# Performance work log

Hardware: AMD Instinct MI355X
Metric: run time of the kernel (lower is better)

## Reference

```python
import jax, jax.numpy as jnp
import numpy as np

B, S, D, H, F = 2, 2048, 1024, 16, 4096
HD = D // H
EPS = 1e-5
NEG = -1e9


def _layernorm(x, g, b):
    mu = jnp.mean(x, axis=-1, keepdims=True)
    var = jnp.mean((x - mu) ** 2, axis=-1, keepdims=True)
    return (x - mu) * jax.lax.rsqrt(var + EPS) * g + b


def _attention(x, wq, wk, wv, wo, bo):
    b, s, d = x.shape
    q = (x @ wq).reshape(b, s, H, HD).transpose(0, 2, 1, 3)  # [b,h,s,hd]
    k = (x @ wk).reshape(b, s, H, HD).transpose(0, 2, 1, 3)
    v = (x @ wv).reshape(b, s, H, HD).transpose(0, 2, 1, 3)
    scores = jnp.einsum('bhqd,bhkd->bhqk', q, k) / (HD ** 0.5)
    # Faithful to source bug: masked_fill(mask == 0, -1e9) where mask = triu(diag=1)
    # -> positions with k <= q (lower triangle incl. diagonal) are filled with -1e9.
    lower = jnp.tril(jnp.ones((s, s), dtype=bool))
    scores = jnp.where(lower, NEG, scores)
    w = jax.nn.softmax(scores, axis=-1)
    o = jnp.einsum('bhqk,bhkd->bhqd', w, v)
    o = o.transpose(0, 2, 1, 3).reshape(b, s, d)
    return o @ wo + bo


def _ffn(x, w1, b1, w2, b2):
    return jax.nn.gelu(x @ w1 + b1, approximate=False) @ w2 + b2


def setup_inputs() -> dict:
    key = jax.random.key(0)
    ks = jax.random.split(key, 10)
    s = 0.02
    return {
        'x': jax.random.normal(ks[0], (B, S, D), jnp.float32),
        'wq': jax.random.normal(ks[1], (D, D), jnp.float32) * s,
        'wk': jax.random.normal(ks[2], (D, D), jnp.float32) * s,
        'wv': jax.random.normal(ks[3], (D, D), jnp.float32) * s,
        'wo': jax.random.normal(ks[4], (D, D), jnp.float32) * s,
        'bo': jnp.zeros((D,), jnp.float32),
        'ln1_g': jnp.ones((D,), jnp.float32),
        'ln1_b': jnp.zeros((D,), jnp.float32),
        'ln2_g': jnp.ones((D,), jnp.float32),
        'ln2_b': jnp.zeros((D,), jnp.float32),
        'w1': jax.random.normal(ks[5], (D, F), jnp.float32) * s,
        'b1': jnp.zeros((F,), jnp.float32),
        'w2': jax.random.normal(ks[6], (F, D), jnp.float32) * s,
        'b2': jnp.zeros((D,), jnp.float32),
    }


def reference(x, wq, wk, wv, wo, bo, ln1_g, ln1_b, ln2_g, ln2_b, w1, b1, w2, b2):
    shortcut = x
    h = _layernorm(x, ln1_g, ln1_b)
    h = _attention(h, wq, wk, wv, wo, bo)  # dropout = identity (eval)
    h = h + shortcut
    shortcut = h
    h2 = _layernorm(h, ln2_g, ln2_b)
    h2 = _attention(h2, wq, wk, wv, wo, bo)  # same attn module reused, per source
    h2 = _ffn(h2, w1, b1, w2, b2)
    return h2 + shortcut
```

## Files before the change

kernel.cpp:

```cpp
#include <hip/hip_runtime.h>
#include <hip/hip_bf16.h>
#include <math.h>

#define Bz 2
#define Sz 2048
#define Dz 1024
#define Hz 16
#define HDz 64
#define Fz 4096
#define ROWS (Bz*Sz)
#define EPSf 1e-5f
#define NEGf -1e9f
#define SC2f 0.1803368801111204f

typedef __attribute__((ext_vector_type(8))) short short8;
typedef __attribute__((ext_vector_type(4))) float floatx4;

__device__ __forceinline__ unsigned short f2bf(float f){
  __hip_bfloat16 h = __float2bfloat16(f);
  return *(unsigned short*)&h;
}
__device__ __forceinline__ float bf2f(unsigned short u){
  union { unsigned x; float f; } a; a.x = ((unsigned)u) << 16; return a.f;
}

__device__ __forceinline__ float fast_gelu(float x){
  float t  = fabsf(x) * 0.70710678118654752f;
  float kk = __builtin_amdgcn_rcpf(1.0f + 0.3275911f * t);
  float poly = ((((1.061405429f*kk - 1.453152027f)*kk + 1.421413741f)*kk
                 - 0.284496736f)*kk + 0.254829592f)*kk;
  float er = 1.0f - poly * __expf(-t*t);
  er = copysignf(er, x);
  return 0.5f * x * (1.0f + er);
}

__device__ __forceinline__ void gload16(const void* g, void* l){
  __builtin_amdgcn_global_load_lds(
      (const __attribute__((address_space(1))) unsigned int*)g,
      (__attribute__((address_space(3))) unsigned int*)l, 16, 0, 0);
}

__device__ __forceinline__ void bar(){
  asm volatile("" ::: "memory");
  __builtin_amdgcn_s_barrier();
  asm volatile("" ::: "memory");
}
#define WAITV6 asm volatile("s_waitcnt vmcnt(6)" ::: "memory")
#define WAITV0 asm volatile("s_waitcnt vmcnt(0)" ::: "memory")
#define WL0    asm volatile("s_waitcnt lgkmcnt(0)" ::: "memory")

__device__ __forceinline__ void xcd_remap(int& bmblk, int& bnblk){
  int gx = gridDim.x, gy = gridDim.y;
  int id = blockIdx.y * gx + blockIdx.x;
  int xcd = id & 7, local = id >> 3;
  bnblk = local % gx;
  bmblk = xcd * (gy >> 3) + local / gx;
}

__global__ __launch_bounds__(256)
void transpose_cast(const float* __restrict__ W, unsigned short* __restrict__ Wt,
                    int K, int N)
{
  __shared__ unsigned short Ts[32][33];
  int n0 = blockIdx.x*32, k0 = blockIdx.y*32;
  int r = threadIdx.x >> 3, c0 = (threadIdx.x & 7) * 4;
  float4 w4 = *(const float4*)(W + (size_t)(k0+r)*N + n0 + c0);
  Ts[r][c0+0] = f2bf(w4.x); Ts[r][c0+1] = f2bf(w4.y);
  Ts[r][c0+2] = f2bf(w4.z); Ts[r][c0+3] = f2bf(w4.w);
  __syncthreads();
  unsigned v0 = Ts[c0+0][r], v1 = Ts[c0+1][r], v2 = Ts[c0+2][r], v3 = Ts[c0+3][r];
  uint2 p; p.x = v0 | (v1<<16); p.y = v2 | (v3<<16);
  *(uint2*)(Wt + (size_t)(n0+r)*K + k0 + c0) = p;
}

__global__ __launch_bounds__(256)
void transpose_bf(const unsigned short* __restrict__ V, unsigned short* __restrict__ VT)
{
  __shared__ unsigned short Ts[32][33];
  int st = blockIdx.x*32;
  int R0 = blockIdx.y*32;
  int b = R0 >> 10, hd0 = R0 & 1023;
  int r = threadIdx.x >> 3, c0 = (threadIdx.x & 7) * 4;
  uint2 w = *(const uint2*)(V + (size_t)(b*Sz + st + r)*Dz + hd0 + c0);
  Ts[r][c0+0] = (unsigned short)(w.x & 0xffff);
  Ts[r][c0+1] = (unsigned short)(w.x >> 16);
  Ts[r][c0+2] = (unsigned short)(w.y & 0xffff);
  Ts[r][c0+3] = (unsigned short)(w.y >> 16);
  __syncthreads();
  unsigned v0 = Ts[c0+0][r], v1 = Ts[c0+1][r], v2 = Ts[c0+2][r], v3 = Ts[c0+3][r];
  uint2 p; p.x = v0 | (v1<<16); p.y = v2 | (v3<<16);
  *(uint2*)(VT + (size_t)(R0+r)*Sz + st + c0) = p;
}

__global__ __launch_bounds__(256)
void ln_kernel(const float* __restrict__ in, const float* __restrict__ gam,
               const float* __restrict__ bet, unsigned short* __restrict__ out)
{
  int row = blockIdx.x, t = threadIdx.x;
  size_t base = (size_t)row * Dz;
  int c0 = t * 4;
  float4 x4 = *(const float4*)(in + base + c0);
  float v[4] = {x4.x, x4.y, x4.z, x4.w};
  float s = v[0]+v[1]+v[2]+v[3];
  #pragma unroll
  for (int off=32; off>0; off>>=1) s += __shfl_down(s, off, 64);
  __shared__ float ws[4];
  int lane = t & 63, wid = t >> 6;
  if (lane == 0) ws[wid] = s;
  __syncthreads();
  float mu = (ws[0]+ws[1]+ws[2]+ws[3]) * (1.0f/Dz);
  __syncthreads();
  float d0=v[0]-mu, d1=v[1]-mu, d2=v[2]-mu, d3=v[3]-mu;
  float s2 = d0*d0+d1*d1+d2*d2+d3*d3;
  #pragma unroll
  for (int off=32; off>0; off>>=1) s2 += __shfl_down(s2, off, 64);
  if (lane == 0) ws[wid] = s2;
  __syncthreads();
  float var = (ws[0]+ws[1]+ws[2]+ws[3]) * (1.0f/Dz);
  float rstd = rsqrtf(var + EPSf);
  float4 g4 = *(const float4*)(gam + c0);
  float4 b4 = *(const float4*)(bet + c0);
  unsigned r0 = f2bf((v[0]-mu)*rstd*g4.x + b4.x);
  unsigned r1 = f2bf((v[1]-mu)*rstd*g4.y + b4.y);
  unsigned r2 = f2bf((v[2]-mu)*rstd*g4.z + b4.z);
  unsigned r3 = f2bf((v[3]-mu)*rstd*g4.w + b4.w);
  uint2 p; p.x = r0 | (r1<<16); p.y = r2 | (r3<<16);
  *(uint2*)(out + base + c0) = p;
}

#define STG_A(buf, half, k0) { \
  _Pragma("unroll") for (int c_=0;c_<2;c_++){ \
    int sg_ = c_*8 + wave; \
    int row0_ = ((sg_>>3)<<7) + ((sg_&7)<<3) + ((half)<<6); \
    gload16(pA[half][c_] + (k0), &As[buf][row0_*64]); } }

#define STG_B(buf, jh, k0) { \
  _Pragma("unroll") for (int c_=0;c_<2;c_++){ \
    int sg_ = c_*8 + wave; int rho0_ = sg_<<3; \
    gload16(pB[jh][c_] + (k0), &Bs[buf][jh][rho0_*64]); } }

#define READ_A4(dst, buf, ihalf) { \
  _Pragma("unroll") for (int ii_=0; ii_<4; ++ii_){ \
    int row_ = wm*128 + ((ihalf)*4+ii_)*16 + l15; \
    _Pragma("unroll") for (int ks_=0; ks_<2; ++ks_){ \
      int slot_ = (ks_*4+quad) ^ (l15&7); \
      dst[ii_][ks_] = *(const short8*)&As[buf][row_*64 + slot_*8]; } } }

#define READ_B2(dst, buf, jh) { \
  _Pragma("unroll") for (int jl_=0; jl_<2; ++jl_){ \
    int rho_ = wn*32 + jl_*16 + l15; \
    _Pragma("unroll") for (int ks_=0; ks_<2; ++ks_){ \
      int slot_ = (ks_*4+quad) ^ (l15&7); \
      dst[jl_][ks_] = *(const short8*)&Bs[buf][jh][rho_*64 + slot_*8]; } } }

#define MFMA_PH(IH, JH, AF, BF) { \
  __builtin_amdgcn_s_setprio(1); \
  _Pragma("unroll") for (int ii_=0; ii_<4; ++ii_){ \
    _Pragma("unroll") for (int jl_=0; jl_<2; ++jl_){ \
      floatx4 c_ = acc[(IH)*4+ii_][(JH)*2+jl_]; \
      c_ = __builtin_amdgcn_mfma_f32_16x16x32_bf16(AF[ii_][0], BF[jl_][0], c_, 0,0,0); \
      c_ = __builtin_amdgcn_mfma_f32_16x16x32_bf16(AF[ii_][1], BF[jl_][1], c_, 0,0,0); \
      acc[(IH)*4+ii_][(JH)*2+jl_] = c_; } } \
  __builtin_amdgcn_s_setprio(0); }

__global__ __launch_bounds__(512, 2)
void gemm256(const unsigned short* __restrict__ A,
             const unsigned short* __restrict__ Bt,
             const float* __restrict__ bias, const float* __restrict__ res,
             float* __restrict__ outf, unsigned short* __restrict__ outb,
             int M, int N, int K, int lda, int ldb, int act, int qkvmode)
{
  __shared__ unsigned short As[2][256*64];
  __shared__ unsigned short Bs[2][2][128*64];

  int t = threadIdx.x;
  int wave = t >> 6, lane = t & 63;
  int l15 = lane & 15, quad = lane >> 4;
  int wm = wave >> 2, wn = wave & 3;

  int nN = gridDim.x, nM = gridDim.y;
  int id = blockIdx.y * nN + blockIdx.x;
  int xcd = id & 7, local = id >> 3;
  int bnblk = local % nN;
  int bmblk = xcd * (nM >> 3) + local / nN;
  int bm = bmblk * 256, bn = bnblk * 256;

  if (gridDim.z > 1){
    A    += (size_t)blockIdx.z * K;
    Bt   += (size_t)blockIdx.z * K;
    outf += (size_t)blockIdx.z * ((size_t)M * N);
  }

  int lrow = lane >> 3;
  int lcol = ((lane & 7) ^ (lane >> 3)) * 8;

  const unsigned short* pA[2][2];
  const unsigned short* pB[2][2];
  #pragma unroll
  for (int half=0; half<2; half++)
    #pragma unroll
    for (int c=0;c<2;c++){
      int sg = c*8 + wave;
      int row0 = ((sg>>3)<<7) + ((sg&7)<<3) + (half<<6);
      pA[half][c] = A + (size_t)(bm + row0 + lrow)*lda + lcol;
    }
  #pragma unroll
  for (int jh=0; jh<2; jh++)
    #pragma unroll
    for (int c=0;c<2;c++){
      int sg = c*8 + wave;
      int rho0 = sg<<3;
      int gn = ((rho0>>5)<<6) + (jh<<5) + (rho0&31);
      pB[jh][c] = Bt + (size_t)(bn + gn + lrow)*ldb + lcol;
    }

  floatx4 acc[8][4];
  #pragma unroll
  for (int i=0;i<8;i++)
    #pragma unroll
    for (int j=0;j<4;j++) acc[i][j] = (floatx4){0.f,0.f,0.f,0.f};

  STG_A(0, 0, 0);  STG_A(0, 1, 0);
  STG_B(0, 0, 0);  STG_B(0, 1, 0);
  STG_A(1, 0, 64); STG_A(1, 1, 64);
  STG_B(1, 0, 64);
  WAITV6;
  bar();

  int NKT = K >> 6;
  int nIter = NKT >> 1;
  for (int it = 0; it < nIter; ++it){
    bool more = (it + 1 < nIter);
    int k0B  = (2*it+1) << 6;
    int k0A2 = (2*it+2) << 6;
    int k0B2 = (2*it+3) << 6;
    short8 aLo[4][2], aHi[4][2], bcur[2][2];

    READ_A4(aLo, 0, 0);
    READ_B2(bcur, 0, 0);
    STG_B(1, 1, k0B);
    bar(); WL0;
    MFMA_PH(0, 0, aLo, bcur);
    bar();

    READ_A4(aHi, 0, 1);
    READ_B2(bcur, 0, 0);
    if (more) STG_A(0, 0, k0A2);
    bar(); WL0;
    MFMA_PH(1, 0, aHi, bcur);
    bar();

    READ_B2(bcur, 0, 1);
    if (more) STG_A(0, 1, k0A2);
    bar(); WL0;
    MFMA_PH(0, 1, aLo, bcur);
    bar();

    if (more) { STG_B(0, 0, k0A2); WAITV6; }
    else      { WAITV0; }
    bar();
    MFMA_PH(1, 1, aHi, bcur);
    bar();

    READ_A4(aLo, 1, 0);
    READ_B2(bcur, 1, 0);
    if (more) STG_B(0, 1, k0A2);
    bar(); WL0;
    MFMA_PH(0, 0, aLo, bcur);
    bar();

    READ_A4(aHi, 1, 1);
    READ_B2(bcur, 1, 0);
    if (more) STG_A(1, 0, k0B2);
    bar(); WL0;
    MFMA_PH(1, 0, aHi, bcur);
    bar();

    READ_B2(bcur, 1, 1);
    if (more) STG_A(1, 1, k0B2);
    bar(); WL0;
    MFMA_PH(0, 1, aLo, bcur);
    bar();

    if (more) { STG_B(1, 0, k0B2); WAITV6; }
    bar();
    MFMA_PH(1, 1, aHi, bcur);
    bar();
  }

  float bj[4];
  #pragma unroll
  for (int j=0;j<4;j++) bj[j] = bias ? bias[bn + wn*64 + j*16 + l15] : 0.f;

  size_t selbase = 0; int ncol = N; int bnl = bn;
  if (qkvmode){ selbase = (size_t)(bn >> 10) * ((size_t)M * 1024); ncol = 1024; bnl = bn & 1023; }

  #pragma unroll
  for (int i=0;i<8;i++){
    int row0 = bm + wm*128 + i*16 + quad*4;
    #pragma unroll
    for (int r=0;r<4;r++){
      size_t rowoff = selbase + (size_t)(row0 + r) * ncol;
      #pragma unroll
      for (int j=0;j<4;j++){
        float v = acc[i][j][r] + bj[j];
        if (act) v = fast_gelu(v);
        size_t off = rowoff + bnl + wn*64 + j*16 + l15;
        if (res) v += res[off];
        if (outf) outf[off] = v;
        else      outb[off] = f2bf(v);
      }
    }
  }
}

__global__ __launch_bounds__(256)
void gemm_n64(const unsigned short* __restrict__ A,
              const unsigned short* __restrict__ Bt,
              const float* __restrict__ bias, const float* __restrict__ res,
              float* __restrict__ outf, unsigned short* __restrict__ outb,
              int M, int N, int K)
{
  __shared__ unsigned short As[2][128*64];
  __shared__ unsigned short Bs[2][64*64];
  int t = threadIdx.x;
  int bmblk, bnblk; xcd_remap(bmblk, bnblk);
  int bm = bmblk * 128, bn = bnblk * 64;
  int wave = t >> 6, lane = t & 63;
  int l15 = lane & 15, quad = lane >> 4;
  int arow = lane >> 3;
  int acbg = ((lane & 7) ^ arow) * 8;
  const unsigned short* gA = A  + (size_t)(bm + wave*32 + arow)*K + acbg;
  const unsigned short* gB = Bt + (size_t)(bn + wave*16 + arow)*K + acbg;

  floatx4 acc[2][4];
  #pragma unroll
  for (int i=0;i<2;i++)
    #pragma unroll
    for (int j=0;j<4;j++) acc[i][j] = (floatx4){0.f,0.f,0.f,0.f};

  int swr = (l15 & 7);

  {
    unsigned short* lA = &As[0][wave*32*64];
    unsigned short* lB = &Bs[0][wave*16*64];
    gload16(gA,                 lA);
    gload16(gA + (size_t)8*K,   lA + 8*64);
    gload16(gA + (size_t)16*K,  lA + 16*64);
    gload16(gA + (size_t)24*K,  lA + 24*64);
    gload16(gB,                 lB);
    gload16(gB + (size_t)8*K,   lB + 8*64);
  }

  int nIter = K >> 6;
  for (int it = 0; it < nIter; ++it) {
    __syncthreads();
    int cur = it & 1;
    if (it + 1 < nIter) {
      int k1 = (it+1) << 6;
      unsigned short* lA = &As[cur^1][wave*32*64];
      unsigned short* lB = &Bs[cur^1][wave*16*64];
      gload16(gA + k1,                 lA);
      gload16(gA + k1 + (size_t)8*K,   lA + 8*64);
      gload16(gA + k1 + (size_t)16*K,  lA + 16*64);
      gload16(gA + k1 + (size_t)24*K,  lA + 24*64);
      gload16(gB + k1,                 lB);
      gload16(gB + k1 + (size_t)8*K,   lB + 8*64);
    }
    const unsigned short* Ac = As[cur];
    const unsigned short* Bc = Bs[cur];
    #pragma unroll
    for (int ks=0; ks<2; ++ks){
      short8 af[2], bf[4];
      #pragma unroll
      for (int i=0;i<2;i++)
        af[i] = *(const short8*)&Ac[(wave*32 + i*16 + l15)*64 + ((ks*4 + quad) ^ swr)*8];
      #pragma unroll
      for (int j=0;j<4;j++)
        bf[j] = *(const short8*)&Bc[(j*16 + l15)*64 + ((ks*4 + quad) ^ swr)*8];
      #pragma unroll
      for (int i=0;i<2;i++)
        #pragma unroll
        for (int j=0;j<4;j++)
          acc[i][j] = __builtin_amdgcn_mfma_f32_16x16x32_bf16(af[i], bf[j], acc[i][j], 0, 0, 0);
    }
  }

  float bj[4];
  #pragma unroll
  for (int j=0;j<4;j++) bj[j] = bias ? bias[bn + j*16 + l15] : 0.f;

  #pragma unroll
  for (int i=0;i<2;i++){
    int row0 = bm + wave*32 + i*16 + quad*4;
    #pragma unroll
    for (int r=0;r<4;r++){
      size_t rowoff = (size_t)(row0 + r) * N;
      #pragma unroll
      for (int j=0;j<4;j++){
        float v = acc[i][j][r] + bj[j];
        size_t off = rowoff + bn + j*16 + l15;
        if (res) v += res[off];
        if (outf) outf[off] = v;
        else      outb[off] = f2bf(v);
      }
    }
  }
}

__global__ __launch_bounds__(256)
void reduce4(const float* __restrict__ part, const float* __restrict__ bias,
             const float* __restrict__ res, float* __restrict__ out)
{
  const size_t NN = (size_t)ROWS * Dz;
  size_t i = ((size_t)blockIdx.x * 256 + threadIdx.x) * 4;
  float4 a = *(const float4*)(part + i);
  float4 b = *(const float4*)(part + NN + i);
  float4 c = *(const float4*)(part + 2*NN + i);
  float4 d = *(const float4*)(part + 3*NN + i);
  float4 r = *(const float4*)(res + i);
  int col = threadIdx.x * 4;
  float4 g = *(const float4*)(bias + col);
  float4 o;
  o.x = a.x+b.x+c.x+d.x + g.x + r.x;
  o.y = a.y+b.y+c.y+d.y + g.y + r.y;
  o.z = a.z+b.z+c.z+d.z + g.z + r.z;
  o.w = a.w+b.w+c.w+d.w + g.w + r.w;
  *(float4*)(out + i) = o;
}

__global__ __launch_bounds__(256)
void vmean_kernel(const unsigned short* __restrict__ v, float* __restrict__ vm)
{
  int h = blockIdx.x, b = blockIdx.y;
  int t = threadIdx.x, d = t & 63, seg = t >> 6;
  float s = 0.f;
  for (int i=0;i<512;i++){
    int srow = seg*512 + i;
    s += bf2f(v[((size_t)(b*Sz + srow))*Dz + h*HDz + d]);
  }
  __shared__ float red[4][64];
  red[seg][d] = s;
  __syncthreads();
  if (seg == 0){
    float tot = red[0][d]+red[1][d]+red[2][d]+red[3][d];
    vm[(b*Hz + h)*HDz + d] = tot * (1.0f/2048.0f);
  }
}

#define ATT_STAGE_KV() { \
    *(uint4*)&Ks[sr*64 + ((kc2  ) ^ ksw)*8] = pk0; \
    *(uint4*)&Ks[sr*64 + ((kc2+1) ^ ksw)*8] = pk1; \
    *(uint4*)&Vts[vd*128 + (((vk8  )&8) | (((vk8  )^vsw)&7))*8] = pv0; \
    *(uint4*)&Vts[vd*128 + (((vk8+1)&8) | (((vk8+1)^vsw)&7))*8] = pv1; }

#define ATT_PREFETCH(tile) { \
    size_t off0_ = ((size_t)(b*Sz + (tile)*128 + sr))*Dz + h*HDz + sc; \
    pk0 = *(const uint4*)(Kg + off0_); pk1 = *(const uint4*)(Kg + off0_ + 8); \
    int vo_ = (tile)*128 + vc*16; \
    pv0 = *(const uint4*)(vrow + vo_); pv1 = *(const uint4*)(vrow + vo_ + 8); }

#define ATT_COMPUTE(MASKED) { \
  _Pragma("unroll") \
  for (int hh=0; hh<2; ++hh){ \
    floatx4 acc_s[4]; \
    _Pragma("unroll") for (int j=0;j<4;j++) acc_s[j] = (floatx4){0.f,0.f,0.f,0.f}; \
    __builtin_amdgcn_s_setprio(1); \
    _Pragma("unroll") \
    for (int ks=0;ks<2;ks++){ \
      short8 bk[4]; \
      _Pragma("unroll") \
      for (int j=0;j<4;j++) \
        bk[j] = *(const short8*)&Ks[(hh*64 + j*16 + l15)*64 + (((ks*4+quad) ^ (l15&7)))*8]; \
      _Pragma("unroll") \
      for (int j=0;j<4;j++) \
        acc_s[j] = __builtin_amdgcn_mfma_f32_16x16x32_bf16(aq[ks], bk[j], acc_s[j], 0, 0, 0); \
    } \
    __builtin_amdgcn_s_setprio(0); \
    _Pragma("unroll") \
    for (int j=0;j<4;j++){ \
      _Pragma("unroll") \
      for (int r=0;r<4;r++){ \
        float s2 = acc_s[j][r] * SC2f; \
        if (MASKED){ int kloc = hh*64 + j*16 + l15; if (kloc <= qloc + r) s2 = NEGf; } \
        float p = __builtin_amdgcn_exp2f(fminf(s2, 115.41f)); \
        lacc[r] += p; \
        Ps[wave*16 + quad*4 + r][j*16 + l15] = f2bf(p); \
      } \
    } \
    __builtin_amdgcn_s_setprio(1); \
    _Pragma("unroll") \
    for (int ks=0;ks<2;ks++){ \
      short8 ap, bv[4]; \
      ap = *(const short8*)&Ps[wave*16 + l15][ks*32 + quad*8]; \
      _Pragma("unroll") \
      for (int j=0;j<4;j++) \
        bv[j] = *(const short8*)&Vts[(j*16 + l15)*128 + (hh*8 + ((ks*4+quad) ^ (l15&7)))*8]; \
      _Pragma("unroll") \
      for (int j=0;j<4;j++) \
        acc_o[j] = __builtin_amdgcn_mfma_f32_16x16x32_bf16(ap, bv[j], acc_o[j], 0, 0, 0); \
    } \
    __builtin_amdgcn_s_setprio(0); \
  } }

__global__ __launch_bounds__(512, 4)
void attn_mfma(const unsigned short* __restrict__ Qg,
               const unsigned short* __restrict__ Kg,
               const unsigned short* __restrict__ VTg,
               const float* __restrict__ vmean,
               unsigned short* __restrict__ Og)
{
  __shared__ unsigned short Ks[128*64];
  __shared__ unsigned short Vts[64*128];
  __shared__ unsigned short Ps[128][72];

  int t = threadIdx.x;
  int wave = t >> 6, lane = t & 63;
  int l15 = lane & 15, quad = lane >> 4;
  int b = blockIdx.z, h = blockIdx.y;
  int qt = b ? (15 - (int)blockIdx.x) : (int)blockIdx.x;

  {
    int r = t >> 2, c = (t & 3) * 16;
    const unsigned short* qp = Qg + ((size_t)(b*Sz + qt*128 + r))*Dz + h*HDz + c;
    uint4 q0 = *(const uint4*)(qp);
    uint4 q1 = *(const uint4*)(qp + 8);
    *(uint4*)&Ps[r][c]     = q0;
    *(uint4*)&Ps[r][c + 8] = q1;
  }

  int sr = t >> 2, sc = (t & 3) * 16;
  int kc2 = (t & 3) * 2, ksw = sr & 7;
  int vd = t >> 3, vc = t & 7, vsw = vd & 7;
  int vk8 = vc * 2;
  const unsigned short* vrow = VTg + ((size_t)((b*Hz + h)*64 + vd))*Sz;

  uint4 pk0, pk1, pv0, pv1;
  ATT_PREFETCH(qt);

  __syncthreads();
  short8 aq[2];
  aq[0] = *(const short8*)&Ps[wave*16 + l15][quad*8];
  aq[1] = *(const short8*)&Ps[wave*16 + l15][32 + quad*8];

  floatx4 acc_o[4];
  #pragma unroll
  for (int j=0;j<4;j++) acc_o[j] = (floatx4){0.f,0.f,0.f,0.f};
  float lacc[4] = {0.f, 0.f, 0.f, 0.f};

  int qloc = wave*16 + quad*4;

  ATT_STAGE_KV();
  __syncthreads();
  if (qt + 1 < Sz/128) ATT_PREFETCH(qt+1);
  ATT_COMPUTE(1);

  for (int jt2 = qt+1; jt2 < Sz/128; ++jt2){
    __syncthreads();
    ATT_STAGE_KV();
    __syncthreads();
    if (jt2 + 1 < Sz/128) ATT_PREFETCH(jt2+1);
    ATT_COMPUTE(0);
  }

  #pragma unroll
  for (int r=0;r<4;r++){
    float l = lacc[r];
    l += __shfl_xor(l, 1, 64);
    l += __shfl_xor(l, 2, 64);
    l += __shfl_xor(l, 4, 64);
    l += __shfl_xor(l, 8, 64);
    int qrow = qt*128 + wave*16 + quad*4 + r;
    float inv = 1.0f / l;
    size_t rowoff = ((size_t)(b*Sz + qrow))*Dz + h*HDz;
    #pragma unroll
    for (int j=0;j<4;j++){
      float ov = acc_o[j][r] * inv;
      if (qrow == Sz-1) ov = vmean[(b*Hz + h)*HDz + j*16 + l15];
      Og[rowoff + j*16 + l15] = f2bf(ov);
    }
  }
}

extern "C" void kernel_launch(void* const* d_in, const int* in_sizes, int n_in,
                              void* d_out, int out_size, void* d_ws, size_t ws_size,
                              hipStream_t stream)
{
  const float* x    = (const float*)d_in[0];
  const float* wq   = (const float*)d_in[1];
  const float* wk   = (const float*)d_in[2];
  const float* wv   = (const float*)d_in[3];
  const float* wo   = (const float*)d_in[4];
  const float* bo   = (const float*)d_in[5];
  const float* ln1g = (const float*)d_in[6];
  const float* ln1b = (const float*)d_in[7];
  const float* ln2g = (const float*)d_in[8];
  const float* ln2b = (const float*)d_in[9];
  const float* w1   = (const float*)d_in[10];
  const float* b1   = (const float*)d_in[11];
  const float* w2   = (const float*)d_in[12];
  const float* b2   = (const float*)d_in[13];
  float* out = (float*)d_out;

  const size_t MB = 1024*1024;
  char* w = (char*)d_ws;
  float*          trunk = (float*)(w);
  unsigned short* lnb   = (unsigned short*)(w + 16*MB);
  unsigned short* q     = (unsigned short*)(w + 24*MB);
  unsigned short* k     = (unsigned short*)(w + 32*MB);
  unsigned short* v     = (unsigned short*)(w + 40*MB);
  unsigned short* ctx   = (unsigned short*)(w + 48*MB);
  unsigned short* wqkvT = (unsigned short*)(w + 56*MB);
  unsigned short* wqT   = wqkvT;
  unsigned short* wkT   = (unsigned short*)(w + 58*MB);
  unsigned short* wvT   = (unsigned short*)(w + 60*MB);
  unsigned short* woT   = (unsigned short*)(w + 62*MB);
  unsigned short* w1T   = (unsigned short*)(w + 64*MB);
  unsigned short* w2T   = (unsigned short*)(w + 72*MB);
  unsigned short* mid   = (unsigned short*)(w + 24*MB);
  float*          part  = (float*)(w + 80*MB);
  bool splitk = ws_size >= (size_t)144*MB;

  unsigned short* vT    = (unsigned short*)d_out;
  float*          vmean = (float*)((char*)d_out + 8*MB);

  dim3 blk(256), blk512(512);
  transpose_cast<<<dim3(32,32),  blk, 0, stream>>>(wq, wqT, Dz, Dz);
  transpose_cast<<<dim3(32,32),  blk, 0, stream>>>(wk, wkT, Dz, Dz);
  transpose_cast<<<dim3(32,32),  blk, 0, stream>>>(wv, wvT, Dz, Dz);
  transpose_cast<<<dim3(32,32),  blk, 0, stream>>>(wo, woT, Dz, Dz);
  transpose_cast<<<dim3(128,32), blk, 0, stream>>>(w1, w1T, Dz, Fz);
  transpose_cast<<<dim3(32,128), blk, 0, stream>>>(w2, w2T, Fz, Dz);

  dim3 gln(ROWS);
  dim3 gqkv(3*Dz/256, ROWS/256);
  dim3 gf1(Fz/256,  ROWS/256);
  dim3 gn64(Dz/64,  ROWS/128);
  dim3 gattn(Sz/128, Hz, Bz);
  dim3 gvm(Hz, Bz);
  dim3 gvt(Sz/32, Bz*Hz*HDz/32);

  ln_kernel<<<gln, blk, 0, stream>>>(x, ln1g, ln1b, lnb);
  gemm256<<<gqkv, blk512, 0, stream>>>(lnb, wqkvT, nullptr, nullptr, nullptr, q, ROWS, 3*Dz, Dz, Dz, Dz, 0, 1);
  transpose_bf<<<gvt, blk, 0, stream>>>(v, vT);
  vmean_kernel<<<gvm, blk, 0, stream>>>(v, vmean);
  attn_mfma<<<gattn, blk512, 0, stream>>>(q, k, vT, vmean, ctx);
  gemm_n64<<<gn64, blk, 0, stream>>>(ctx, woT, bo, x, trunk, nullptr, ROWS, Dz, Dz);

  ln_kernel<<<gln, blk, 0, stream>>>(trunk, ln2g, ln2b, lnb);
  gemm256<<<gqkv, blk512, 0, stream>>>(lnb, wqkvT, nullptr, nullptr, nullptr, q, ROWS, 3*Dz, Dz, Dz, Dz, 0, 1);
  transpose_bf<<<gvt, blk, 0, stream>>>(v, vT);
  vmean_kernel<<<gvm, blk, 0, stream>>>(v, vmean);
  attn_mfma<<<gattn, blk512, 0, stream>>>(q, k, vT, vmean, ctx);
  gemm_n64<<<gn64, blk, 0, stream>>>(ctx, woT, bo, nullptr, nullptr, lnb, ROWS, Dz, Dz);
  gemm256<<<gf1, blk512, 0, stream>>>(lnb, w1T, b1, nullptr, nullptr, mid, ROWS, Fz, Dz, Dz, Dz, 1, 0);
  if (splitk) {
    gemm256<<<dim3(4,16,4), blk512, 0, stream>>>(mid, w2T, nullptr, nullptr, part, nullptr, ROWS, Dz, Fz/4, Fz, Fz, 0, 0);
    reduce4<<<dim3(4096), blk, 0, stream>>>(part, b2, trunk, out);
  } else {
    gemm_n64<<<gn64, blk, 0, stream>>>(mid, w2T, b2, trunk, out, nullptr, ROWS, Dz, Fz);
  }
}
```

Before: 510.8 us.

## Batch weight transposes, fuse V-mean into V transpose, trim GEMM barriers

Merges the six weight transpose-cast launches into two batched kernels indexed by blockIdx.z. The separate vmean kernel is removed: the V transpose kernel now accumulates per-column sums through shuffles and atomicAdd into a zeroed buffer, and the attention kernel applies the 1/2048 scale itself. In the gemm256 main loop, the trailing barrier after each MFMA phase is dropped, lgkmcnt is waited before the barrier, and the phase order is changed so a B fragment read is reused instead of re-read. The goal is fewer launches and less LDS traffic and synchronisation, at the cost of atomic float nondeterminism and possible LDS write-after-read hazards now that the trailing barriers are gone.

```diff
diff --git a/kernel.cpp b/kernel.cpp
--- a/kernel.cpp
+++ b/kernel.cpp
@@ -57,12 +57,11 @@
   bmblk = xcd * (gy >> 3) + local / gx;
 }
 
-__global__ __launch_bounds__(256)
-void transpose_cast(const float* __restrict__ W, unsigned short* __restrict__ Wt,
-                    int K, int N)
+__device__ __forceinline__ void tc_body(const float* __restrict__ W,
+                                        unsigned short* __restrict__ Wt,
+                                        int K, int N, int n0, int k0)
 {
   __shared__ unsigned short Ts[32][33];
-  int n0 = blockIdx.x*32, k0 = blockIdx.y*32;
   int r = threadIdx.x >> 3, c0 = (threadIdx.x & 7) * 4;
   float4 w4 = *(const float4*)(W + (size_t)(k0+r)*N + n0 + c0);
   Ts[r][c0+0] = f2bf(w4.x); Ts[r][c0+1] = f2bf(w4.y);
@@ -74,7 +73,33 @@
 }
 
 __global__ __launch_bounds__(256)
-void transpose_bf(const unsigned short* __restrict__ V, unsigned short* __restrict__ VT)
+void transpose_qkvo(const float* __restrict__ w0, unsigned short* __restrict__ t0,
+                    const float* __restrict__ w1, unsigned short* __restrict__ t1,
+                    const float* __restrict__ w2, unsigned short* __restrict__ t2,
+                    const float* __restrict__ w3, unsigned short* __restrict__ t3)
+{
+  int z = blockIdx.z;
+  const float* W = z==0 ? w0 : z==1 ? w1 : z==2 ? w2 : w3;
+  unsigned short* T = z==0 ? t0 : z==1 ? t1 : z==2 ? t2 : t3;
+  tc_body(W, T, Dz, Dz, blockIdx.x*32, blockIdx.y*32);
+}
+
+__global__ __launch_bounds__(256)
+void transpose_ffn(const float* __restrict__ w1, unsigned short* __restrict__ w1T,
+                   const float* __restrict__ w2, unsigned short* __restrict__ w2T)
+{
+  int z = blockIdx.z;
+  const float* W = z ? w2 : w1;
+  unsigned short* T = z ? w2T : w1T;
+  int K = z ? Fz : Dz, N = z ? Dz : Fz;
+  int n0 = (z ? blockIdx.y : blockIdx.x) * 32;
+  int k0 = (z ? blockIdx.x : blockIdx.y) * 32;
+  tc_body(W, T, K, N, n0, k0);
+}
+
+__global__ __launch_bounds__(256)
+void transpose_bf(const unsigned short* __restrict__ V, unsigned short* __restrict__ VT,
+                  float* __restrict__ vsum)
 {
   __shared__ unsigned short Ts[32][33];
   int st = blockIdx.x*32;
@@ -90,6 +115,12 @@
   unsigned v0 = Ts[c0+0][r], v1 = Ts[c0+1][r], v2 = Ts[c0+2][r], v3 = Ts[c0+3][r];
   uint2 p; p.x = v0 | (v1<<16); p.y = v2 | (v3<<16);
   *(uint2*)(VT + (size_t)(R0+r)*Sz + st + c0) = p;
+  float s = bf2f((unsigned short)v0) + bf2f((unsigned short)v1)
+          + bf2f((unsigned short)v2) + bf2f((unsigned short)v3);
+  s += __shfl_down(s, 1, 8);
+  s += __shfl_down(s, 2, 8);
+  s += __shfl_down(s, 4, 8);
+  if ((threadIdx.x & 7) == 0) atomicAdd(vsum + R0 + r, s);
 }
 
 __global__ __launch_bounds__(256)
@@ -239,53 +270,43 @@
     READ_A4(aLo, 0, 0);
     READ_B2(bcur, 0, 0);
     STG_B(1, 1, k0B);
-    bar(); WL0;
+    WL0; bar();
     MFMA_PH(0, 0, aLo, bcur);
-    bar();
 
     READ_A4(aHi, 0, 1);
-    READ_B2(bcur, 0, 0);
     if (more) STG_A(0, 0, k0A2);
-    bar(); WL0;
+    WL0; bar();
     MFMA_PH(1, 0, aHi, bcur);
-    bar();
 
     READ_B2(bcur, 0, 1);
     if (more) STG_A(0, 1, k0A2);
-    bar(); WL0;
-    MFMA_PH(0, 1, aLo, bcur);
-    bar();
+    WL0; bar();
+    MFMA_PH(1, 1, aHi, bcur);
 
     if (more) { STG_B(0, 0, k0A2); WAITV6; }
     else      { WAITV0; }
     bar();
-    MFMA_PH(1, 1, aHi, bcur);
-    bar();
+    MFMA_PH(0, 1, aLo, bcur);
 
     READ_A4(aLo, 1, 0);
     READ_B2(bcur, 1, 0);
     if (more) STG_B(0, 1, k0A2);
-    bar(); WL0;
+    WL0; bar();
     MFMA_PH(0, 0, aLo, bcur);
-    bar();
 
     READ_A4(aHi, 1, 1);
-    READ_B2(bcur, 1, 0);
     if (more) STG_A(1, 0, k0B2);
-    bar(); WL0;
+    WL0; bar();
     MFMA_PH(1, 0, aHi, bcur);
-    bar();
 
     READ_B2(bcur, 1, 1);
     if (more) STG_A(1, 1, k0B2);
-    bar(); WL0;
-    MFMA_PH(0, 1, aLo, bcur);
-    bar();
+    WL0; bar();
+    MFMA_PH(1, 1, aHi, bcur);
 
     if (more) { STG_B(1, 0, k0B2); WAITV6; }
     bar();
-    MFMA_PH(1, 1, aHi, bcur);
-    bar();
+    MFMA_PH(0, 1, aLo, bcur);
   }
 
   float bj[4];
@@ -427,25 +448,6 @@
   o.z = a.z+b.z+c.z+d.z + g.z + r.z;
   o.w = a.w+b.w+c.w+d.w + g.w + r.w;
   *(float4*)(out + i) = o;
-}
-
-__global__ __launch_bounds__(256)
-void vmean_kernel(const unsigned short* __restrict__ v, float* __restrict__ vm)
-{
-  int h = blockIdx.x, b = blockIdx.y;
-  int t = threadIdx.x, d = t & 63, seg = t >> 6;
-  float s = 0.f;
-  for (int i=0;i<512;i++){
-    int srow = seg*512 + i;
-    s += bf2f(v[((size_t)(b*Sz + srow))*Dz + h*HDz + d]);
-  }
-  __shared__ float red[4][64];
-  red[seg][d] = s;
-  __syncthreads();
-  if (seg == 0){
-    float tot = red[0][d]+red[1][d]+red[2][d]+red[3][d];
-    vm[(b*Hz + h)*HDz + d] = tot * (1.0f/2048.0f);
-  }
 }
 
 #define ATT_STAGE_KV() { \
@@ -576,7 +578,7 @@
     #pragma unroll
     for (int j=0;j<4;j++){
       float ov = acc_o[j][r] * inv;
-      if (qrow == Sz-1) ov = vmean[(b*Hz + h)*HDz + j*16 + l15];
+      if (qrow == Sz-1) ov = vmean[(b*Hz + h)*HDz + j*16 + l15] * (1.0f/2048.0f);
       Og[rowoff + j*16 + l15] = f2bf(ov);
     }
   }
@@ -625,32 +627,27 @@
   float*          vmean = (float*)((char*)d_out + 8*MB);
 
   dim3 blk(256), blk512(512);
-  transpose_cast<<<dim3(32,32),  blk, 0, stream>>>(wq, wqT, Dz, Dz);
-  transpose_cast<<<dim3(32,32),  blk, 0, stream>>>(wk, wkT, Dz, Dz);
-  transpose_cast<<<dim3(32,32),  blk, 0, stream>>>(wv, wvT, Dz, Dz);
-  transpose_cast<<<dim3(32,32),  blk, 0, stream>>>(wo, woT, Dz, Dz);
-  transpose_cast<<<dim3(128,32), blk, 0, stream>>>(w1, w1T, Dz, Fz);
-  transpose_cast<<<dim3(32,128), blk, 0, stream>>>(w2, w2T, Fz, Dz);
+  transpose_qkvo<<<dim3(32,32,4), blk, 0, stream>>>(wq, wqT, wk, wkT, wv, wvT, wo, woT);
+  transpose_ffn<<<dim3(128,32,2), blk, 0, stream>>>(w1, w1T, w2, w2T);
 
   dim3 gln(ROWS);
   dim3 gqkv(3*Dz/256, ROWS/256);
   dim3 gf1(Fz/256,  ROWS/256);
   dim3 gn64(Dz/64,  ROWS/128);
   dim3 gattn(Sz/128, Hz, Bz);
-  dim3 gvm(Hz, Bz);
   dim3 gvt(Sz/32, Bz*Hz*HDz/32);
 
   ln_kernel<<<gln, blk, 0, stream>>>(x, ln1g, ln1b, lnb);
   gemm256<<<gqkv, blk512, 0, stream>>>(lnb, wqkvT, nullptr, nullptr, nullptr, q, ROWS, 3*Dz, Dz, Dz, Dz, 0, 1);
-  transpose_bf<<<gvt, blk, 0, stream>>>(v, vT);
-  vmean_kernel<<<gvm, blk, 0, stream>>>(v, vmean);
+  hipMemsetAsync(vmean, 0, 2048*sizeof(float), stream);
+  transpose_bf<<<gvt, blk, 0, stream>>>(v, vT, vmean);
   attn_mfma<<<gattn, blk512, 0, stream>>>(q, k, vT, vmean, ctx);
   gemm_n64<<<gn64, blk, 0, stream>>>(ctx, woT, bo, x, trunk, nullptr, ROWS, Dz, Dz);
 
   ln_kernel<<<gln, blk, 0, stream>>>(trunk, ln2g, ln2b, lnb);
   gemm256<<<gqkv, blk512, 0, stream>>>(lnb, wqkvT, nullptr, nullptr, nullptr, q, ROWS, 3*Dz, Dz, Dz, Dz, 0, 1);
-  transpose_bf<<<gvt, blk, 0, stream>>>(v, vT);
-  vmean_kernel<<<gvm, blk, 0, stream>>>(v, vmean);
+  hipMemsetAsync(vmean, 0, 2048*sizeof(float), stream);
+  transpose_bf<<<gvt, blk, 0, stream>>>(v, vT, vmean);
   attn_mfma<<<gattn, blk512, 0, stream>>>(q, k, vT, vmean, ctx);
   gemm_n64<<<gn64, blk, 0, stream>>>(ctx, woT, bo, nullptr, nullptr, lnb, ROWS, Dz, Dz);
   gemm256<<<gf1, blk512, 0, stream>>>(lnb, w1T, b1, nullptr, nullptr, mid, ROWS, Fz, Dz, Dz, Dz, 1, 0);
```

After: 453.0 us. 1.13x faster.
